# Optimization experiments

Hardware: AMD Instinct MI355X
Metric: run time of the kernel (lower is better)

Reference implementation:

```python
import jax, jax.numpy as jnp
import numpy as np

N = 100000

def _gcn_norm(edge_index, n):
    row, col = edge_index[0], edge_index[1]
    deg = jnp.zeros((n,), jnp.float32).at[col].add(1.0)
    dinv = jnp.where(deg > 0, jax.lax.rsqrt(jnp.maximum(deg, 1.0)), 0.0)
    return dinv[row] * dinv[col]


def _arma_conv(x, row, col, norm, init_w, w, root_w, bias):
    # x: [N, Fin]; init_w: [K, Fin, F]; w: [T-1, K, F, F]; root_w: [T, K, Fin, F]; bias: [T, K, 1, F]
    out = jnp.einsum('nf,kfg->kng', x, init_w)  # [K, N, F]
    T = root_w.shape[0]
    for t in range(T):
        if t > 0:
            out = jnp.einsum('kng,kgh->knh', out, w[t - 1])
        msg = out[:, row, :] * norm[None, :, None]          # [K, E, F] gather
        out = jnp.zeros_like(out).at[:, col, :].add(msg)    # scatter-add to targets
        out = out + jnp.einsum('nf,kfg->kng', x, root_w[t]) + bias[t]
        out = jax.nn.relu(out)
    return out.mean(axis=0)  # average over stacks K


def setup_inputs() -> dict:
    key = jax.random.key(0)
    ks = jax.random.split(key, 12)
    E, Fin, H, C, K = 1600000, 128, 64, 41, 2
    s = 0.1
    return {
        'x': jax.random.normal(ks[0], (N, Fin), jnp.float32),
        'edge_index': jax.random.randint(ks[1], (2, E), 0, N, jnp.int64),
        'w1_init': jax.random.normal(ks[2], (K, Fin, H), jnp.float32) * s,
        'w1': jax.random.normal(ks[3], (1, K, H, H), jnp.float32) * s,
        'w1_root': jax.random.normal(ks[4], (2, K, Fin, H), jnp.float32) * s,
        'b1': jax.random.normal(ks[5], (2, K, 1, H), jnp.float32) * s,
        'w2_init': jax.random.normal(ks[6], (K, H, C), jnp.float32) * s,
        'w2': jax.random.normal(ks[7], (1, K, C, C), jnp.float32) * s,
        'w2_root': jax.random.normal(ks[8], (2, K, H, C), jnp.float32) * s,
        'b2': jax.random.normal(ks[9], (2, K, 1, C), jnp.float32) * s,
    }


def reference(x, edge_index, w1_init, w1, w1_root, b1, w2_init, w2, w2_root, b2):
    row, col = edge_index[0], edge_index[1]
    norm = _gcn_norm(edge_index, N)
    h = jax.nn.relu(_arma_conv(x, row, col, norm, w1_init, w1, w1_root, b1))
    # F.dropout is identity in eval mode
    h = _arma_conv(h, row, col, norm, w2_init, w2, w2_root, b2)
    return jax.nn.log_softmax(h, axis=1)
```

## Files before the change

kernel.cpp:

```cpp
#include <hip/hip_runtime.h>
#include <math.h>

#define TPB 256
typedef unsigned short ushort_t;
typedef unsigned int uint_t;
typedef __attribute__((ext_vector_type(8))) short bf16x8;
typedef __attribute__((ext_vector_type(4))) float f32x4;

__device__ __forceinline__ float bf2f(ushort_t h) {
    return __uint_as_float(((uint_t)h) << 16);
}
__device__ __forceinline__ ushort_t f2bf(float f) {
    uint_t u = __float_as_uint(f);
    u += 0x7fff + ((u >> 16) & 1);
    return (ushort_t)(u >> 16);
}
__device__ __forceinline__ uint_t pack2(float x, float y) {
    return (uint_t)f2bf(x) | ((uint_t)f2bf(y) << 16);
}

__global__ void rank_kernel(const int* __restrict__ col, int* __restrict__ cnt,
                            int* __restrict__ pos, int E) {
    int e = blockIdx.x * blockDim.x + threadIdx.x;
    if (e < E) pos[e] = atomicAdd(&cnt[col[e]], 1);
}

__global__ void scan_block(const int* __restrict__ cnt, int* __restrict__ incl,
                           int* __restrict__ bsum, int N) {
    __shared__ int s[TPB];
    int i = blockIdx.x * TPB + threadIdx.x;
    s[threadIdx.x] = (i < N) ? cnt[i] : 0;
    __syncthreads();
    for (int d = 1; d < TPB; d <<= 1) {
        int t = (threadIdx.x >= d) ? s[threadIdx.x - d] : 0;
        __syncthreads();
        s[threadIdx.x] += t;
        __syncthreads();
    }
    if (i < N) incl[i] = s[threadIdx.x];
    if (threadIdx.x == TPB - 1) bsum[blockIdx.x] = s[TPB - 1];
}

__global__ void scan_bsums(int* __restrict__ bsum, int nb) {
    __shared__ int s[512];
    int t = threadIdx.x;
    int v = (t < nb) ? bsum[t] : 0;
    s[t] = v;
    __syncthreads();
    for (int d = 1; d < 512; d <<= 1) {
        int u = (t >= d) ? s[t - d] : 0;
        __syncthreads();
        s[t] += u;
        __syncthreads();
    }
    if (t < nb) bsum[t] = s[t] - v;
}

__global__ void finalize_csr(const int* __restrict__ incl, const int* __restrict__ bsum,
                             const int* __restrict__ cnt, int* __restrict__ rowstart,
                             float* __restrict__ dinv, int N) {
    int i = blockIdx.x * TPB + threadIdx.x;
    if (i < N) {
        rowstart[i + 1] = incl[i] + bsum[blockIdx.x];
        int d = cnt[i];
        dinv[i] = (d > 0) ? rsqrtf((float)d) : 0.0f;
    }
    if (i == 0) rowstart[0] = 0;
}

__global__ void fill_csr(const int* __restrict__ row, const int* __restrict__ col,
                         const int* __restrict__ rowstart, const int* __restrict__ pos,
                         int* __restrict__ srcidx, int E) {
    int e = blockIdx.x * blockDim.x + threadIdx.x;
    if (e < E) srcidx[rowstart[col[e]] + pos[e]] = row[e];
}

__global__ void cvt4_kernel(const float4* __restrict__ src, uint2* __restrict__ dst, int n4) {
    int i = blockIdx.x * blockDim.x + threadIdx.x;
    if (i < n4) {
        float4 v = src[i];
        dst[i] = make_uint2(pack2(v.x, v.y), pack2(v.z, v.w));
    }
}

#define SWZ_A 32768
#define SWZ_B 24576
#define SWZ_C 12288
#define SWZ_D 12288
__global__ void swz_all(const float* __restrict__ w1_init, const float* __restrict__ w1,
                        const float* __restrict__ w1_root, const float* __restrict__ w2_init,
                        const float* __restrict__ w2, const float* __restrict__ w2_root,
                        short* __restrict__ dst) {
    int idx = blockIdx.x * blockDim.x + threadIdx.x;
    int region, base, CH, CT;
    if (idx < SWZ_A)                          { region = 0; base = 0; CH = 4; CT = 8; }
    else if (idx < SWZ_A + SWZ_B)             { region = 1; base = SWZ_A; CH = 6; CT = 4; }
    else if (idx < SWZ_A + SWZ_B + SWZ_C)     { region = 2; base = SWZ_A + SWZ_B; CH = 2; CT = 6; }
    else if (idx < SWZ_A + SWZ_B + SWZ_C + SWZ_D)
                                              { region = 3; base = SWZ_A + SWZ_B + SWZ_C; CH = 4; CT = 3; }
    else return;
    int r = idx - base;
    int j = r & 7, ln = (r >> 3) & 63;
    int rest = r >> 9;
    int ct = rest % CT, c = (rest / CT) % CH, k = rest / (CT * CH);
    int col = ct * 16 + (ln & 15);
    int kl = (ln >> 4) * 8 + j;
    float v = 0.0f;
    if (region == 0) {
        int kk = c * 32 + kl;
        if (col < 64)       v = w1_init[((size_t)k * 128 + kk) * 64 + col];
        else                v = w1_root[((size_t)k * 128 + kk) * 64 + (col - 64)];
    } else if (region == 1) {
        if (c < 2) { int kk = c * 32 + kl;        v = w1[((size_t)k * 64 + kk) * 64 + col]; }
        else       { int kk = (c - 2) * 32 + kl;  v = w1_root[((size_t)(2 + k) * 128 + kk) * 64 + col]; }
    } else if (region == 2) {
        int kk = c * 32 + kl;
        if (col < 48) { if (col < 41)            v = w2_init[((size_t)k * 64 + kk) * 41 + col]; }
        else          { int c2 = col - 48; if (c2 < 41) v = w2_root[((size_t)k * 64 + kk) * 41 + c2]; }
    } else {
        if (c < 2) { int kk = c * 32 + kl;       if (kk < 41 && col < 41) v = w2[((size_t)k * 41 + kk) * 41 + col]; }
        else       { int kk = (c - 2) * 32 + kl; if (col < 41)            v = w2_root[((size_t)(2 + k) * 64 + kk) * 41 + col]; }
    }
    dst[(size_t)base + r] = (short)f2bf(v);
}

template<int CT, int CTA, int CH>
__global__ __launch_bounds__(256)
void gemm_t0(const ushort_t* __restrict__ s2, int s2s, const short* __restrict__ fragbuf,
             const float* __restrict__ biasB, int FB, int N,
             uint_t* __restrict__ pre, uint_t* __restrict__ outH) {
    constexpr int PP = (CT - CTA) * 8;
    constexpr int PA = CTA * 8;
    const int k = blockIdx.y;
    const int n0 = blockIdx.x * 128;
    const int t = threadIdx.x;
    const int w = t >> 6, lane = t & 63, quad = lane >> 4, lr = lane & 15;
    const short* fb = fragbuf + (size_t)k * CH * CT * 512;

    __shared__ short lds_b[CH * CT * 512];
    {
        constexpr int CHUNKS = CH * CT * 64;
#pragma unroll
        for (int i = 0; i < (CHUNKS + 255) / 256; ++i) {
            int idx = i * 256 + t;
            if (CHUNKS % 256 == 0 || idx < CHUNKS)
                *(bf16x8*)&lds_b[idx * 8] = *(const bf16x8*)&fb[(size_t)idx * 8];
        }
    }
    __syncthreads();

    int r0 = n0 + w * 32 + lr;
    int m0 = r0 < N ? r0 : N - 1;
    int m1 = (r0 + 16) < N ? (r0 + 16) : N - 1;

    f32x4 acc[2][CT];
#pragma unroll
    for (int rt = 0; rt < 2; ++rt)
#pragma unroll
        for (int ct = 0; ct < CT; ++ct) acc[rt][ct] = (f32x4){0.f, 0.f, 0.f, 0.f};

#pragma unroll
    for (int c = 0; c < CH; ++c) {
        int off = c * 32 + quad * 8;
        bf16x8 a0 = *(const bf16x8*)&s2[(size_t)m0 * s2s + off];
        bf16x8 a1 = *(const bf16x8*)&s2[(size_t)m1 * s2s + off];
#pragma unroll
        for (int ct = 0; ct < CT; ++ct) {
            bf16x8 b = *(const bf16x8*)&lds_b[((size_t)c * CT + ct) * 512 + lane * 8];
            acc[0][ct] = __builtin_amdgcn_mfma_f32_16x16x32_bf16(a0, b, acc[0][ct], 0, 0, 0);
            acc[1][ct] = __builtin_amdgcn_mfma_f32_16x16x32_bf16(a1, b, acc[1][ct], 0, 0, 0);
        }
    }

#pragma unroll
    for (int rt = 0; rt < 2; ++rt) {
#pragma unroll
        for (int i = 0; i < 4; ++i) {
            int n = n0 + w * 32 + rt * 16 + quad * 4 + i;
            if (n >= N) continue;
#pragma unroll
            for (int ct = 0; ct < CT; ++ct) {
                int col = ct * 16 + lr;
                float v = acc[rt][ct][i];
                if (ct >= CTA) {
                    int c2 = col - CTA * 16;
                    if (c2 < FB) v += biasB[(size_t)k * FB + c2];
                }
                float vn = __shfl_xor(v, 1);
                uint_t p = pack2(v, vn);
                uint_t p2 = __shfl_xor(p, 2);
                if (!(lr & 3)) {
                    if (ct < CTA) {
                        *(uint2*)&outH[((size_t)n * 2 + k) * PA + (col >> 1)] = make_uint2(p, p2);
                    } else {
                        int c2 = col - CTA * 16;
                        *(uint2*)&pre[((size_t)n * 2 + k) * PP + (c2 >> 1)] = make_uint2(p, p2);
                    }
                }
            }
        }
    }
}

__global__ __launch_bounds__(256)
void gemm_t1_l1(const ushort_t* __restrict__ s1, const ushort_t* __restrict__ xh,
                const short* __restrict__ fragbuf, const float* __restrict__ bias,
                int N, uint_t* __restrict__ hhU) {
    constexpr int CT = 4, CH = 6;
    const int n0 = blockIdx.x * 128;
    const int t = threadIdx.x;
    const int w = t >> 6, lane = t & 63, quad = lane >> 4, lr = lane & 15;

    __shared__ short lds_b[2 * CH * CT * 512];
    {
        constexpr int CHUNKS = 2 * CH * CT * 64;
#pragma unroll
        for (int i = 0; i < CHUNKS / 256; ++i) {
            int idx = i * 256 + t;
            *(bf16x8*)&lds_b[idx * 8] = *(const bf16x8*)&fragbuf[(size_t)idx * 8];
        }
    }
    __syncthreads();

    int r0 = n0 + w * 32 + lr;
    int m0 = r0 < N ? r0 : N - 1;
    int m1 = (r0 + 16) < N ? (r0 + 16) : N - 1;

    f32x4 acc[2][2][CT];
#pragma unroll
    for (int k = 0; k < 2; ++k)
#pragma unroll
        for (int rt = 0; rt < 2; ++rt)
#pragma unroll
            for (int ct = 0; ct < CT; ++ct) acc[k][rt][ct] = (f32x4){0.f, 0.f, 0.f, 0.f};

#pragma unroll
    for (int c = 0; c < CH; ++c) {
        bf16x8 a0[2], a1[2];
        if (c < 2) {
            int off = c * 32 + quad * 8;
#pragma unroll
            for (int k = 0; k < 2; ++k) {
                a0[k] = *(const bf16x8*)&s1[((size_t)m0 * 2 + k) * 64 + off];
                a1[k] = *(const bf16x8*)&s1[((size_t)m1 * 2 + k) * 64 + off];
            }
        } else {
            int off = (c - 2) * 32 + quad * 8;
            a0[0] = a0[1] = *(const bf16x8*)&xh[(size_t)m0 * 128 + off];
            a1[0] = a1[1] = *(const bf16x8*)&xh[(size_t)m1 * 128 + off];
        }
#pragma unroll
        for (int k = 0; k < 2; ++k) {
#pragma unroll
            for (int ct = 0; ct < CT; ++ct) {
                bf16x8 b = *(const bf16x8*)&lds_b[(((size_t)k * CH + c) * CT + ct) * 512 + lane * 8];
                acc[k][0][ct] = __builtin_amdgcn_mfma_f32_16x16x32_bf16(a0[k], b, acc[k][0][ct], 0, 0, 0);
                acc[k][1][ct] = __builtin_amdgcn_mfma_f32_16x16x32_bf16(a1[k], b, acc[k][1][ct], 0, 0, 0);
            }
        }
    }

#pragma unroll
    for (int rt = 0; rt < 2; ++rt) {
#pragma unroll
        for (int i = 0; i < 4; ++i) {
            int n = n0 + w * 32 + rt * 16 + quad * 4 + i;
            if (n >= N) continue;
#pragma unroll
            for (int ct = 0; ct < CT; ++ct) {
                int col = ct * 16 + lr;
                float v0 = fmaxf(acc[0][rt][ct][i] + bias[col], 0.0f);
                float v1 = fmaxf(acc[1][rt][ct][i] + bias[64 + col], 0.0f);
                float m = 0.5f * (v0 + v1);
                float mn = __shfl_xor(m, 1);
                uint_t p = pack2(m, mn);
                uint_t p2 = __shfl_xor(p, 2);
                if (!(lr & 3)) *(uint2*)&hhU[(size_t)n * 32 + (col >> 1)] = make_uint2(p, p2);
            }
        }
    }
}

__global__ __launch_bounds__(256)
void gemm_t1_l2(const ushort_t* __restrict__ s1, const ushort_t* __restrict__ hh,
                const short* __restrict__ fragbuf, const float* __restrict__ bias,
                int N, float* __restrict__ out) {
    constexpr int CT = 3, CH = 4;
    const int n0 = blockIdx.x * 128;
    const int t = threadIdx.x;
    const int w = t >> 6, lane = t & 63, quad = lane >> 4, lr = lane & 15;

    __shared__ short lds_b[2 * CH * CT * 512];
    {
        constexpr int CHUNKS = 2 * CH * CT * 64;
#pragma unroll
        for (int i = 0; i < CHUNKS / 256; ++i) {
            int idx = i * 256 + t;
            *(bf16x8*)&lds_b[idx * 8] = *(const bf16x8*)&fragbuf[(size_t)idx * 8];
        }
    }
    __syncthreads();

    int r0 = n0 + w * 32 + lr;
    int m0 = r0 < N ? r0 : N - 1;
    int m1 = (r0 + 16) < N ? (r0 + 16) : N - 1;

    f32x4 acc[2][2][CT];
#pragma unroll
    for (int k = 0; k < 2; ++k)
#pragma unroll
        for (int rt = 0; rt < 2; ++rt)
#pragma unroll
            for (int ct = 0; ct < CT; ++ct) acc[k][rt][ct] = (f32x4){0.f, 0.f, 0.f, 0.f};

#pragma unroll
    for (int c = 0; c < CH; ++c) {
        bf16x8 a0[2], a1[2];
        if (c < 2) {
            int off = c * 32 + quad * 8;
#pragma unroll
            for (int k = 0; k < 2; ++k) {
                a0[k] = *(const bf16x8*)&s1[((size_t)m0 * 2 + k) * 48 + off];
                a1[k] = *(const bf16x8*)&s1[((size_t)m1 * 2 + k) * 48 + off];
            }
        } else {
            int off = (c - 2) * 32 + quad * 8;
            a0[0] = a0[1] = *(const bf16x8*)&hh[(size_t)m0 * 64 + off];
            a1[0] = a1[1] = *(const bf16x8*)&hh[(size_t)m1 * 64 + off];
        }
#pragma unroll
        for (int k = 0; k < 2; ++k) {
#pragma unroll
            for (int ct = 0; ct < CT; ++ct) {
                bf16x8 b = *(const bf16x8*)&lds_b[(((size_t)k * CH + c) * CT + ct) * 512 + lane * 8];
                acc[k][0][ct] = __builtin_amdgcn_mfma_f32_16x16x32_bf16(a0[k], b, acc[k][0][ct], 0, 0, 0);
                acc[k][1][ct] = __builtin_amdgcn_mfma_f32_16x16x32_bf16(a1[k], b, acc[k][1][ct], 0, 0, 0);
            }
        }
    }

#pragma unroll
    for (int rt = 0; rt < 2; ++rt) {
#pragma unroll
        for (int i = 0; i < 4; ++i) {
            int n = n0 + w * 32 + rt * 16 + quad * 4 + i;
            float m[CT];
            float mx = -1e30f;
#pragma unroll
            for (int ct = 0; ct < CT; ++ct) {
                int col = ct * 16 + lr;
                float b0 = (col < 41) ? bias[col] : 0.0f;
                float b1v = (col < 41) ? bias[41 + col] : 0.0f;
                float v0 = fmaxf(acc[0][rt][ct][i] + b0, 0.0f);
                float v1 = fmaxf(acc[1][rt][ct][i] + b1v, 0.0f);
                m[ct] = 0.5f * (v0 + v1);
                if (col < 41) mx = fmaxf(mx, m[ct]);
            }
#pragma unroll
            for (int msk = 1; msk < 16; msk <<= 1) mx = fmaxf(mx, __shfl_xor(mx, msk));
            float s = 0.0f;
#pragma unroll
            for (int ct = 0; ct < CT; ++ct) {
                int col = ct * 16 + lr;
                if (col < 41) s += __expf(m[ct] - mx);
            }
#pragma unroll
            for (int msk = 1; msk < 16; msk <<= 1) s += __shfl_xor(s, msk);
            float ls = __logf(s);
            if (n < N) {
#pragma unroll
                for (int ct = 0; ct < CT; ++ct) {
                    int col = ct * 16 + lr;
                    if (col < 41) out[(size_t)n * 41 + col] = m[ct] - mx - ls;
                }
            }
        }
    }
}

template<int PAIRS>
__global__ __launch_bounds__(256)
void gather(const int* __restrict__ rowstart, const int* __restrict__ srcidx,
            const float* __restrict__ dinv, const uint_t* __restrict__ msg,
            const uint_t* __restrict__ pre, uint_t* __restrict__ outH, int N) {
    int gt = blockIdx.x * 256 + threadIdx.x;
    int n = gt >> 6, lane = gt & 63;
    if (n >= N) return;
    int k, pair;
    if (PAIRS == 32) { k = lane >> 5; pair = lane & 31; }
    else { k = lane / PAIRS; pair = lane - k * PAIRS; }
    if (k >= 2) return;
    int beg = rowstart[n], end = rowstart[n + 1];
    float dn = dinv[n];
    float ax = 0.0f, ay = 0.0f;
    int e = beg;
    for (; e + 7 < end; e += 8) {
        int s[8];
        float w[8];
        uint_t m[8];
#pragma unroll
        for (int j = 0; j < 8; ++j) s[j] = srcidx[e + j];
#pragma unroll
        for (int j = 0; j < 8; ++j) w[j] = dinv[s[j]];
#pragma unroll
        for (int j = 0; j < 8; ++j) m[j] = msg[((size_t)s[j] * 2 + k) * PAIRS + pair];
#pragma unroll
        for (int j = 0; j < 8; ++j) {
            float ww = w[j] * dn;
            ax = fmaf(bf2f((ushort_t)m[j]), ww, ax);
            ay = fmaf(bf2f((ushort_t)(m[j] >> 16)), ww, ay);
        }
    }
    if (e + 3 < end) {
        int s[4];
        float w[4];
        uint_t m[4];
#pragma unroll
        for (int j = 0; j < 4; ++j) s[j] = srcidx[e + j];
#pragma unroll
        for (int j = 0; j < 4; ++j) w[j] = dinv[s[j]];
#pragma unroll
        for (int j = 0; j < 4; ++j) m[j] = msg[((size_t)s[j] * 2 + k) * PAIRS + pair];
#pragma unroll
        for (int j = 0; j < 4; ++j) {
            float ww = w[j] * dn;
            ax = fmaf(bf2f((ushort_t)m[j]), ww, ax);
            ay = fmaf(bf2f((ushort_t)(m[j] >> 16)), ww, ay);
        }
        e += 4;
    }
    for (; e < end; ++e) {
        int s0 = srcidx[e];
        float ww = dinv[s0] * dn;
        uint_t m0 = msg[((size_t)s0 * 2 + k) * PAIRS + pair];
        ax = fmaf(bf2f((ushort_t)m0), ww, ax);
        ay = fmaf(bf2f((ushort_t)(m0 >> 16)), ww, ay);
    }
    size_t o = ((size_t)n * 2 + k) * PAIRS + pair;
    if (pre) {
        uint_t p = pre[o];
        ax = fmaxf(ax + bf2f((ushort_t)p), 0.0f);
        ay = fmaxf(ay + bf2f((ushort_t)(p >> 16)), 0.0f);
    }
    outH[o] = pack2(ax, ay);
}

extern "C" void kernel_launch(void* const* d_in, const int* in_sizes, int n_in,
                              void* d_out, int out_size, void* d_ws, size_t ws_size,
                              hipStream_t stream) {
    const float* x       = (const float*)d_in[0];
    const int*   ei      = (const int*)  d_in[1];
    const float* w1_init = (const float*)d_in[2];
    const float* w1      = (const float*)d_in[3];
    const float* w1_root = (const float*)d_in[4];
    const float* b1      = (const float*)d_in[5];
    const float* w2_init = (const float*)d_in[6];
    const float* w2      = (const float*)d_in[7];
    const float* w2_root = (const float*)d_in[8];
    const float* b2      = (const float*)d_in[9];

    const int Fin1 = 128;
    int N = in_sizes[0] / Fin1;
    int E = in_sizes[1] / 2;
    const int* row = ei;
    const int* col = ei + E;

    char* ws = (char*)d_ws;
    size_t off = 0;
    auto carve = [&](size_t bytes) -> void* {
        void* p = ws + off;
        off += (bytes + 255) & ~(size_t)255;
        return p;
    };
    int nblkN = (N + TPB - 1) / TPB;
    int*      cnt      = (int*)     carve((size_t)N * 4);
    int*      incl     = (int*)     carve((size_t)N * 4);
    int*      rowstart = (int*)     carve((size_t)(N + 1) * 4);
    int*      bsum     = (int*)     carve((size_t)nblkN * 4);
    float*    dinv     = (float*)   carve((size_t)N * 4);
    int*      pos      = (int*)     carve((size_t)E * 4);
    int*      srcidx   = (int*)     carve((size_t)E * 4);
    short*    swz      = (short*)   carve((size_t)(SWZ_A + SWZ_B + SWZ_C + SWZ_D) * 2);
    ushort_t* xh       = (ushort_t*)carve((size_t)N * 128 * 2);
    ushort_t* hh       = (ushort_t*)carve((size_t)N * 64 * 2);
    ushort_t* b16A     = (ushort_t*)carve((size_t)N * 2 * 64 * 2);
    ushort_t* b16B     = (ushort_t*)carve((size_t)N * 2 * 64 * 2);
    uint_t*   pre      = (uint_t*)  carve((size_t)N * 2 * 32 * 4);

    hipMemsetAsync(cnt, 0, (size_t)N * 4, stream);
    rank_kernel <<<(E + TPB - 1) / TPB, TPB, 0, stream>>>(col, cnt, pos, E);
    scan_block  <<<nblkN, TPB, 0, stream>>>(cnt, incl, bsum, N);
    scan_bsums  <<<1, 512, 0, stream>>>(bsum, nblkN);
    finalize_csr<<<nblkN, TPB, 0, stream>>>(incl, bsum, cnt, rowstart, dinv, N);
    fill_csr    <<<(E + TPB - 1) / TPB, TPB, 0, stream>>>(row, col, rowstart, pos, srcidx, E);

    int swztot = SWZ_A + SWZ_B + SWZ_C + SWZ_D;
    swz_all<<<(swztot + TPB - 1) / TPB, TPB, 0, stream>>>(w1_init, w1, w1_root,
                                                          w2_init, w2, w2_root, swz);
    int nx4 = N * 128 / 4;
    cvt4_kernel<<<(nx4 + TPB - 1) / TPB, TPB, 0, stream>>>((const float4*)x, (uint2*)xh, nx4);

    dim3 gg2((N + 127) / 128, 2);
    dim3 gg1((N + 127) / 128, 1);
    int ggb = (N * 64 + TPB - 1) / TPB;
    const short* swzA = swz;
    const short* swzB = swz + SWZ_A;
    const short* swzC = swz + SWZ_A + SWZ_B;
    const short* swzD = swz + SWZ_A + SWZ_B + SWZ_C;

    gemm_t0<8, 4, 4><<<gg2, TPB, 0, stream>>>(xh, 128, swzA, b1, 64, N, pre, (uint_t*)b16A);
    gather<32><<<ggb, TPB, 0, stream>>>(rowstart, srcidx, dinv, (const uint_t*)b16A,
                                        pre, (uint_t*)b16B, N);
    gather<32><<<ggb, TPB, 0, stream>>>(rowstart, srcidx, dinv, (const uint_t*)b16B,
                                        nullptr, (uint_t*)b16A, N);
    gemm_t1_l1<<<gg1, TPB, 0, stream>>>(b16A, xh, swzB, b1 + 2 * 64, N, (uint_t*)hh);

    gemm_t0<6, 3, 2><<<gg2, TPB, 0, stream>>>(hh, 64, swzC, b2, 41, N, pre, (uint_t*)b16A);
    gather<24><<<ggb, TPB, 0, stream>>>(rowstart, srcidx, dinv, (const uint_t*)b16A,
                                        pre, (uint_t*)b16B, N);
    gather<24><<<ggb, TPB, 0, stream>>>(rowstart, srcidx, dinv, (const uint_t*)b16B,
                                        nullptr, (uint_t*)b16A, N);
    gemm_t1_l2<<<gg1, TPB, 0, stream>>>(b16A, hh, swzD, b2 + 2 * 41, N, (float*)d_out);
}
```

Measured before the change: 606.2 us.

## Pad CSR rows to multiples of four and pre-scale messages by source dinv

Rows of the CSR adjacency are padded to a multiple of four with a dummy source index N that points at a zeroed tail row, so the gather can load indices as int4 and drop its scalar tail loops. The source-side normalisation dinv[s] is moved into the producer (the GEMM epilogue or the previous gather's output), which removes the per-edge dinv lookup and multiply. The per-edge rank is also stored as ushort, and the GEMMs hoist their A-operand global loads ahead of the LDS staging and get occupancy hints. In exchange it adds a padding kernel, extra memsets and a larger srcidx buffer. The ushort rank assumes in-degree below 65536, and the change in rounding order could shift bf16 results slightly.

```diff
diff --git a/kernel.cpp b/kernel.cpp
--- a/kernel.cpp
+++ b/kernel.cpp
@@ -20,16 +20,16 @@
 }
 
 __global__ void rank_kernel(const int* __restrict__ col, int* __restrict__ cnt,
-                            int* __restrict__ pos, int E) {
+                            unsigned short* __restrict__ pos, int E) {
     int e = blockIdx.x * blockDim.x + threadIdx.x;
-    if (e < E) pos[e] = atomicAdd(&cnt[col[e]], 1);
+    if (e < E) pos[e] = (unsigned short)atomicAdd(&cnt[col[e]], 1);
 }
 
 __global__ void scan_block(const int* __restrict__ cnt, int* __restrict__ incl,
                            int* __restrict__ bsum, int N) {
     __shared__ int s[TPB];
     int i = blockIdx.x * TPB + threadIdx.x;
-    s[threadIdx.x] = (i < N) ? cnt[i] : 0;
+    s[threadIdx.x] = (i < N) ? ((cnt[i] + 3) & ~3) : 0;
     __syncthreads();
     for (int d = 1; d < TPB; d <<= 1) {
         int t = (threadIdx.x >= d) ? s[threadIdx.x - d] : 0;
@@ -69,10 +69,18 @@
 }
 
 __global__ void fill_csr(const int* __restrict__ row, const int* __restrict__ col,
-                         const int* __restrict__ rowstart, const int* __restrict__ pos,
+                         const int* __restrict__ rowstart, const unsigned short* __restrict__ pos,
                          int* __restrict__ srcidx, int E) {
     int e = blockIdx.x * blockDim.x + threadIdx.x;
-    if (e < E) srcidx[rowstart[col[e]] + pos[e]] = row[e];
+    if (e < E) srcidx[rowstart[col[e]] + (int)pos[e]] = row[e];
+}
+
+__global__ void pad_csr(const int* __restrict__ rowstart, const int* __restrict__ cnt,
+                        int* __restrict__ srcidx, int N) {
+    int i = blockIdx.x * blockDim.x + threadIdx.x;
+    if (i >= N) return;
+    int b = rowstart[i] + cnt[i], en = rowstart[i + 1];
+    for (int e = b; e < en; ++e) srcidx[e] = N;
 }
 
 __global__ void cvt4_kernel(const float4* __restrict__ src, uint2* __restrict__ dst, int n4) {
@@ -125,10 +133,10 @@
 }
 
 template<int CT, int CTA, int CH>
-__global__ __launch_bounds__(256)
+__global__ __launch_bounds__(256, 4)
 void gemm_t0(const ushort_t* __restrict__ s2, int s2s, const short* __restrict__ fragbuf,
-             const float* __restrict__ biasB, int FB, int N,
-             uint_t* __restrict__ pre, uint_t* __restrict__ outH) {
+             const float* __restrict__ biasB, const float* __restrict__ dinv,
+             int FB, int N, uint_t* __restrict__ pre, uint_t* __restrict__ outH) {
     constexpr int PP = (CT - CTA) * 8;
     constexpr int PA = CTA * 8;
     const int k = blockIdx.y;
@@ -137,6 +145,18 @@
     const int w = t >> 6, lane = t & 63, quad = lane >> 4, lr = lane & 15;
     const short* fb = fragbuf + (size_t)k * CH * CT * 512;
 
+    int r0 = n0 + w * 32 + lr;
+    int m0 = r0 < N ? r0 : N - 1;
+    int m1 = (r0 + 16) < N ? (r0 + 16) : N - 1;
+
+    bf16x8 a0v[CH], a1v[CH];
+#pragma unroll
+    for (int c = 0; c < CH; ++c) {
+        int off = c * 32 + quad * 8;
+        a0v[c] = *(const bf16x8*)&s2[(size_t)m0 * s2s + off];
+        a1v[c] = *(const bf16x8*)&s2[(size_t)m1 * s2s + off];
+    }
+
     __shared__ short lds_b[CH * CT * 512];
     {
         constexpr int CHUNKS = CH * CT * 64;
@@ -149,10 +169,6 @@
     }
     __syncthreads();
 
-    int r0 = n0 + w * 32 + lr;
-    int m0 = r0 < N ? r0 : N - 1;
-    int m1 = (r0 + 16) < N ? (r0 + 16) : N - 1;
-
     f32x4 acc[2][CT];
 #pragma unroll
     for (int rt = 0; rt < 2; ++rt)
@@ -161,14 +177,11 @@
 
 #pragma unroll
     for (int c = 0; c < CH; ++c) {
-        int off = c * 32 + quad * 8;
-        bf16x8 a0 = *(const bf16x8*)&s2[(size_t)m0 * s2s + off];
-        bf16x8 a1 = *(const bf16x8*)&s2[(size_t)m1 * s2s + off];
 #pragma unroll
         for (int ct = 0; ct < CT; ++ct) {
             bf16x8 b = *(const bf16x8*)&lds_b[((size_t)c * CT + ct) * 512 + lane * 8];
-            acc[0][ct] = __builtin_amdgcn_mfma_f32_16x16x32_bf16(a0, b, acc[0][ct], 0, 0, 0);
-            acc[1][ct] = __builtin_amdgcn_mfma_f32_16x16x32_bf16(a1, b, acc[1][ct], 0, 0, 0);
+            acc[0][ct] = __builtin_amdgcn_mfma_f32_16x16x32_bf16(a0v[c], b, acc[0][ct], 0, 0, 0);
+            acc[1][ct] = __builtin_amdgcn_mfma_f32_16x16x32_bf16(a1v[c], b, acc[1][ct], 0, 0, 0);
         }
     }
 
@@ -178,11 +191,14 @@
         for (int i = 0; i < 4; ++i) {
             int n = n0 + w * 32 + rt * 16 + quad * 4 + i;
             if (n >= N) continue;
+            float dnv = dinv[n];
 #pragma unroll
             for (int ct = 0; ct < CT; ++ct) {
                 int col = ct * 16 + lr;
                 float v = acc[rt][ct][i];
-                if (ct >= CTA) {
+                if (ct < CTA) {
+                    v *= dnv;
+                } else {
                     int c2 = col - CTA * 16;
                     if (c2 < FB) v += biasB[(size_t)k * FB + c2];
                 }
@@ -202,7 +218,7 @@
     }
 }
 
-__global__ __launch_bounds__(256)
+__global__ __launch_bounds__(256, 3)
 void gemm_t1_l1(const ushort_t* __restrict__ s1, const ushort_t* __restrict__ xh,
                 const short* __restrict__ fragbuf, const float* __restrict__ bias,
                 int N, uint_t* __restrict__ hhU) {
@@ -211,6 +227,28 @@
     const int t = threadIdx.x;
     const int w = t >> 6, lane = t & 63, quad = lane >> 4, lr = lane & 15;
 
+    int r0 = n0 + w * 32 + lr;
+    int m0 = r0 < N ? r0 : N - 1;
+    int m1 = (r0 + 16) < N ? (r0 + 16) : N - 1;
+
+    bf16x8 s0a[2][2], s1a[2][2];
+    bf16x8 x0a[4], x1a[4];
+#pragma unroll
+    for (int c = 0; c < 2; ++c) {
+        int off = c * 32 + quad * 8;
+#pragma unroll
+        for (int kk = 0; kk < 2; ++kk) {
+            s0a[c][kk] = *(const bf16x8*)&s1[((size_t)m0 * 2 + kk) * 64 + off];
+            s1a[c][kk] = *(const bf16x8*)&s1[((size_t)m1 * 2 + kk) * 64 + off];
+        }
+    }
+#pragma unroll
+    for (int c = 0; c < 4; ++c) {
+        int off = c * 32 + quad * 8;
+        x0a[c] = *(const bf16x8*)&xh[(size_t)m0 * 128 + off];
+        x1a[c] = *(const bf16x8*)&xh[(size_t)m1 * 128 + off];
+    }
+
     __shared__ short lds_b[2 * CH * CT * 512];
     {
         constexpr int CHUNKS = 2 * CH * CT * 64;
@@ -222,10 +260,6 @@
     }
     __syncthreads();
 
-    int r0 = n0 + w * 32 + lr;
-    int m0 = r0 < N ? r0 : N - 1;
-    int m1 = (r0 + 16) < N ? (r0 + 16) : N - 1;
-
     f32x4 acc[2][2][CT];
 #pragma unroll
     for (int k = 0; k < 2; ++k)
@@ -236,26 +270,15 @@
 
 #pragma unroll
     for (int c = 0; c < CH; ++c) {
-        bf16x8 a0[2], a1[2];
-        if (c < 2) {
-            int off = c * 32 + quad * 8;
-#pragma unroll
-            for (int k = 0; k < 2; ++k) {
-                a0[k] = *(const bf16x8*)&s1[((size_t)m0 * 2 + k) * 64 + off];
-                a1[k] = *(const bf16x8*)&s1[((size_t)m1 * 2 + k) * 64 + off];
-            }
-        } else {
-            int off = (c - 2) * 32 + quad * 8;
-            a0[0] = a0[1] = *(const bf16x8*)&xh[(size_t)m0 * 128 + off];
-            a1[0] = a1[1] = *(const bf16x8*)&xh[(size_t)m1 * 128 + off];
-        }
 #pragma unroll
         for (int k = 0; k < 2; ++k) {
+            bf16x8 a0 = (c < 2) ? s0a[c][k] : x0a[c - 2];
+            bf16x8 a1 = (c < 2) ? s1a[c][k] : x1a[c - 2];
 #pragma unroll
             for (int ct = 0; ct < CT; ++ct) {
                 bf16x8 b = *(const bf16x8*)&lds_b[(((size_t)k * CH + c) * CT + ct) * 512 + lane * 8];
-                acc[k][0][ct] = __builtin_amdgcn_mfma_f32_16x16x32_bf16(a0[k], b, acc[k][0][ct], 0, 0, 0);
-                acc[k][1][ct] = __builtin_amdgcn_mfma_f32_16x16x32_bf16(a1[k], b, acc[k][1][ct], 0, 0, 0);
+                acc[k][0][ct] = __builtin_amdgcn_mfma_f32_16x16x32_bf16(a0, b, acc[k][0][ct], 0, 0, 0);
+                acc[k][1][ct] = __builtin_amdgcn_mfma_f32_16x16x32_bf16(a1, b, acc[k][1][ct], 0, 0, 0);
             }
         }
     }
@@ -281,7 +304,7 @@
     }
 }
 
-__global__ __launch_bounds__(256)
+__global__ __launch_bounds__(256, 3)
 void gemm_t1_l2(const ushort_t* __restrict__ s1, const ushort_t* __restrict__ hh,
                 const short* __restrict__ fragbuf, const float* __restrict__ bias,
                 int N, float* __restrict__ out) {
@@ -290,6 +313,28 @@
     const int t = threadIdx.x;
     const int w = t >> 6, lane = t & 63, quad = lane >> 4, lr = lane & 15;
 
+    int r0 = n0 + w * 32 + lr;
+    int m0 = r0 < N ? r0 : N - 1;
+    int m1 = (r0 + 16) < N ? (r0 + 16) : N - 1;
+
+    bf16x8 s0a[2][2], s1a[2][2];
+    bf16x8 h0a[2], h1a[2];
+#pragma unroll
+    for (int c = 0; c < 2; ++c) {
+        int off = c * 32 + quad * 8;
+#pragma unroll
+        for (int kk = 0; kk < 2; ++kk) {
+            s0a[c][kk] = *(const bf16x8*)&s1[((size_t)m0 * 2 + kk) * 48 + off];
+            s1a[c][kk] = *(const bf16x8*)&s1[((size_t)m1 * 2 + kk) * 48 + off];
+        }
+    }
+#pragma unroll
+    for (int c = 0; c < 2; ++c) {
+        int off = c * 32 + quad * 8;
+        h0a[c] = *(const bf16x8*)&hh[(size_t)m0 * 64 + off];
+        h1a[c] = *(const bf16x8*)&hh[(size_t)m1 * 64 + off];
+    }
+
     __shared__ short lds_b[2 * CH * CT * 512];
     {
         constexpr int CHUNKS = 2 * CH * CT * 64;
@@ -301,10 +346,6 @@
     }
     __syncthreads();
 
-    int r0 = n0 + w * 32 + lr;
-    int m0 = r0 < N ? r0 : N - 1;
-    int m1 = (r0 + 16) < N ? (r0 + 16) : N - 1;
-
     f32x4 acc[2][2][CT];
 #pragma unroll
     for (int k = 0; k < 2; ++k)
@@ -315,26 +356,15 @@
 
 #pragma unroll
     for (int c = 0; c < CH; ++c) {
-        bf16x8 a0[2], a1[2];
-        if (c < 2) {
-            int off = c * 32 + quad * 8;
-#pragma unroll
-            for (int k = 0; k < 2; ++k) {
-                a0[k] = *(const bf16x8*)&s1[((size_t)m0 * 2 + k) * 48 + off];
-                a1[k] = *(const bf16x8*)&s1[((size_t)m1 * 2 + k) * 48 + off];
-            }
-        } else {
-            int off = (c - 2) * 32 + quad * 8;
-            a0[0] = a0[1] = *(const bf16x8*)&hh[(size_t)m0 * 64 + off];
-            a1[0] = a1[1] = *(const bf16x8*)&hh[(size_t)m1 * 64 + off];
-        }
 #pragma unroll
         for (int k = 0; k < 2; ++k) {
+            bf16x8 a0 = (c < 2) ? s0a[c][k] : h0a[c - 2];
+            bf16x8 a1 = (c < 2) ? s1a[c][k] : h1a[c - 2];
 #pragma unroll
             for (int ct = 0; ct < CT; ++ct) {
                 bf16x8 b = *(const bf16x8*)&lds_b[(((size_t)k * CH + c) * CT + ct) * 512 + lane * 8];
-                acc[k][0][ct] = __builtin_amdgcn_mfma_f32_16x16x32_bf16(a0[k], b, acc[k][0][ct], 0, 0, 0);
-                acc[k][1][ct] = __builtin_amdgcn_mfma_f32_16x16x32_bf16(a1[k], b, acc[k][1][ct], 0, 0, 0);
+                acc[k][0][ct] = __builtin_amdgcn_mfma_f32_16x16x32_bf16(a0, b, acc[k][0][ct], 0, 0, 0);
+                acc[k][1][ct] = __builtin_amdgcn_mfma_f32_16x16x32_bf16(a1, b, acc[k][1][ct], 0, 0, 0);
             }
         }
     }
@@ -378,7 +408,7 @@
     }
 }
 
-template<int PAIRS>
+template<int PAIRS, bool SCALE_OUT>
 __global__ __launch_bounds__(256)
 void gather(const int* __restrict__ rowstart, const int* __restrict__ srcidx,
             const float* __restrict__ dinv, const uint_t* __restrict__ msg,
@@ -390,58 +420,54 @@
     if (PAIRS == 32) { k = lane >> 5; pair = lane & 31; }
     else { k = lane / PAIRS; pair = lane - k * PAIRS; }
     if (k >= 2) return;
+    const int STR = 2 * PAIRS;
+    const uint_t lo = (uint_t)(k * PAIRS + pair);
     int beg = rowstart[n], end = rowstart[n + 1];
     float dn = dinv[n];
-    float ax = 0.0f, ay = 0.0f;
+    size_t o = (size_t)n * STR + lo;
+    uint_t p = 0;
+    if (pre) p = pre[o];
+
+    float ax0 = 0.f, ax1 = 0.f, ay0 = 0.f, ay1 = 0.f;
     int e = beg;
-    for (; e + 7 < end; e += 8) {
-        int s[8];
-        float w[8];
-        uint_t m[8];
-#pragma unroll
-        for (int j = 0; j < 8; ++j) s[j] = srcidx[e + j];
-#pragma unroll
-        for (int j = 0; j < 8; ++j) w[j] = dinv[s[j]];
-#pragma unroll
-        for (int j = 0; j < 8; ++j) m[j] = msg[((size_t)s[j] * 2 + k) * PAIRS + pair];
-#pragma unroll
-        for (int j = 0; j < 8; ++j) {
-            float ww = w[j] * dn;
-            ax = fmaf(bf2f((ushort_t)m[j]), ww, ax);
-            ay = fmaf(bf2f((ushort_t)(m[j] >> 16)), ww, ay);
-        }
-    }
-    if (e + 3 < end) {
-        int s[4];
-        float w[4];
-        uint_t m[4];
-#pragma unroll
-        for (int j = 0; j < 4; ++j) s[j] = srcidx[e + j];
-#pragma unroll
-        for (int j = 0; j < 4; ++j) w[j] = dinv[s[j]];
-#pragma unroll
-        for (int j = 0; j < 4; ++j) m[j] = msg[((size_t)s[j] * 2 + k) * PAIRS + pair];
-#pragma unroll
-        for (int j = 0; j < 4; ++j) {
-            float ww = w[j] * dn;
-            ax = fmaf(bf2f((ushort_t)m[j]), ww, ax);
-            ay = fmaf(bf2f((ushort_t)(m[j] >> 16)), ww, ay);
-        }
-        e += 4;
-    }
-    for (; e < end; ++e) {
-        int s0 = srcidx[e];
-        float ww = dinv[s0] * dn;
-        uint_t m0 = msg[((size_t)s0 * 2 + k) * PAIRS + pair];
-        ax = fmaf(bf2f((ushort_t)m0), ww, ax);
-        ay = fmaf(bf2f((ushort_t)(m0 >> 16)), ww, ay);
-    }
-    size_t o = ((size_t)n * 2 + k) * PAIRS + pair;
+    for (; e + 8 <= end; e += 8) {
+        int4 sa = *(const int4*)&srcidx[e];
+        int4 sb = *(const int4*)&srcidx[e + 4];
+        uint_t m0 = msg[(uint_t)(sa.x * STR) + lo];
+        uint_t m1 = msg[(uint_t)(sa.y * STR) + lo];
+        uint_t m2 = msg[(uint_t)(sa.z * STR) + lo];
+        uint_t m3 = msg[(uint_t)(sa.w * STR) + lo];
+        uint_t m4 = msg[(uint_t)(sb.x * STR) + lo];
+        uint_t m5 = msg[(uint_t)(sb.y * STR) + lo];
+        uint_t m6 = msg[(uint_t)(sb.z * STR) + lo];
+        uint_t m7 = msg[(uint_t)(sb.w * STR) + lo];
+        ax0 += __uint_as_float(m0 << 16); ay0 += __uint_as_float(m0 & 0xffff0000u);
+        ax1 += __uint_as_float(m1 << 16); ay1 += __uint_as_float(m1 & 0xffff0000u);
+        ax0 += __uint_as_float(m2 << 16); ay0 += __uint_as_float(m2 & 0xffff0000u);
+        ax1 += __uint_as_float(m3 << 16); ay1 += __uint_as_float(m3 & 0xffff0000u);
+        ax0 += __uint_as_float(m4 << 16); ay0 += __uint_as_float(m4 & 0xffff0000u);
+        ax1 += __uint_as_float(m5 << 16); ay1 += __uint_as_float(m5 & 0xffff0000u);
+        ax0 += __uint_as_float(m6 << 16); ay0 += __uint_as_float(m6 & 0xffff0000u);
+        ax1 += __uint_as_float(m7 << 16); ay1 += __uint_as_float(m7 & 0xffff0000u);
+    }
+    if (e < end) {
+        int4 sa = *(const int4*)&srcidx[e];
+        uint_t m0 = msg[(uint_t)(sa.x * STR) + lo];
+        uint_t m1 = msg[(uint_t)(sa.y * STR) + lo];
+        uint_t m2 = msg[(uint_t)(sa.z * STR) + lo];
+        uint_t m3 = msg[(uint_t)(sa.w * STR) + lo];
+        ax0 += __uint_as_float(m0 << 16); ay0 += __uint_as_float(m0 & 0xffff0000u);
+        ax1 += __uint_as_float(m1 << 16); ay1 += __uint_as_float(m1 & 0xffff0000u);
+        ax0 += __uint_as_float(m2 << 16); ay0 += __uint_as_float(m2 & 0xffff0000u);
+        ax1 += __uint_as_float(m3 << 16); ay1 += __uint_as_float(m3 & 0xffff0000u);
+    }
+    float ax = (ax0 + ax1) * dn;
+    float ay = (ay0 + ay1) * dn;
     if (pre) {
-        uint_t p = pre[o];
         ax = fmaxf(ax + bf2f((ushort_t)p), 0.0f);
         ay = fmaxf(ay + bf2f((ushort_t)(p >> 16)), 0.0f);
     }
+    if (SCALE_OUT) { ax *= dn; ay *= dn; }
     outH[o] = pack2(ax, ay);
 }
 
@@ -478,20 +504,24 @@
     int*      rowstart = (int*)     carve((size_t)(N + 1) * 4);
     int*      bsum     = (int*)     carve((size_t)nblkN * 4);
     float*    dinv     = (float*)   carve((size_t)N * 4);
-    int*      pos      = (int*)     carve((size_t)E * 4);
-    int*      srcidx   = (int*)     carve((size_t)E * 4);
+    unsigned short* pos = (unsigned short*)carve((size_t)E * 2);
+    int*      srcidx   = (int*)     carve((size_t)(E + 3 * (size_t)N + 64) * 4);
     short*    swz      = (short*)   carve((size_t)(SWZ_A + SWZ_B + SWZ_C + SWZ_D) * 2);
     ushort_t* xh       = (ushort_t*)carve((size_t)N * 128 * 2);
     ushort_t* hh       = (ushort_t*)carve((size_t)N * 64 * 2);
-    ushort_t* b16A     = (ushort_t*)carve((size_t)N * 2 * 64 * 2);
-    ushort_t* b16B     = (ushort_t*)carve((size_t)N * 2 * 64 * 2);
+    ushort_t* b16A     = (ushort_t*)carve((size_t)N * 2 * 64 * 2 + 256);
+    ushort_t* b16B     = (ushort_t*)carve((size_t)N * 2 * 64 * 2 + 256);
     uint_t*   pre      = (uint_t*)  carve((size_t)N * 2 * 32 * 4);
+
+    hipMemsetAsync((char*)b16A + (size_t)N * 256, 0, 256, stream);
+    hipMemsetAsync((char*)b16B + (size_t)N * 256, 0, 256, stream);
 
     hipMemsetAsync(cnt, 0, (size_t)N * 4, stream);
     rank_kernel <<<(E + TPB - 1) / TPB, TPB, 0, stream>>>(col, cnt, pos, E);
     scan_block  <<<nblkN, TPB, 0, stream>>>(cnt, incl, bsum, N);
     scan_bsums  <<<1, 512, 0, stream>>>(bsum, nblkN);
     finalize_csr<<<nblkN, TPB, 0, stream>>>(incl, bsum, cnt, rowstart, dinv, N);
+    pad_csr     <<<nblkN, TPB, 0, stream>>>(rowstart, cnt, srcidx, N);
     fill_csr    <<<(E + TPB - 1) / TPB, TPB, 0, stream>>>(row, col, rowstart, pos, srcidx, E);
 
     int swztot = SWZ_A + SWZ_B + SWZ_C + SWZ_D;
@@ -508,17 +538,20 @@
     const short* swzC = swz + SWZ_A + SWZ_B;
     const short* swzD = swz + SWZ_A + SWZ_B + SWZ_C;
 
-    gemm_t0<8, 4, 4><<<gg2, TPB, 0, stream>>>(xh, 128, swzA, b1, 64, N, pre, (uint_t*)b16A);
-    gather<32><<<ggb, TPB, 0, stream>>>(rowstart, srcidx, dinv, (const uint_t*)b16A,
-                                        pre, (uint_t*)b16B, N);
-    gather<32><<<ggb, TPB, 0, stream>>>(rowstart, srcidx, dinv, (const uint_t*)b16B,
-                                        nullptr, (uint_t*)b16A, N);
+    gemm_t0<8, 4, 4><<<gg2, TPB, 0, stream>>>(xh, 128, swzA, b1, dinv, 64, N, pre, (uint_t*)b16A);
+    gather<32, true ><<<ggb, TPB, 0, stream>>>(rowstart, srcidx, dinv, (const uint_t*)b16A,
+                                               pre, (uint_t*)b16B, N);
+    gather<32, false><<<ggb, TPB, 0, stream>>>(rowstart, srcidx, dinv, (const uint_t*)b16B,
+                                               nullptr, (uint_t*)b16A, N);
     gemm_t1_l1<<<gg1, TPB, 0, stream>>>(b16A, xh, swzB, b1 + 2 * 64, N, (uint_t*)hh);
 
-    gemm_t0<6, 3, 2><<<gg2, TPB, 0, stream>>>(hh, 64, swzC, b2, 41, N, pre, (uint_t*)b16A);
-    gather<24><<<ggb, TPB, 0, stream>>>(rowstart, srcidx, dinv, (const uint_t*)b16A,
-                                        pre, (uint_t*)b16B, N);
-    gather<24><<<ggb, TPB, 0, stream>>>(rowstart, srcidx, dinv, (const uint_t*)b16B,
-                                        nullptr, (uint_t*)b16A, N);
+    hipMemsetAsync((char*)b16A + (size_t)N * 192, 0, 192, stream);
+    hipMemsetAsync((char*)b16B + (size_t)N * 192, 0, 192, stream);
+
+    gemm_t0<6, 3, 2><<<gg2, TPB, 0, stream>>>(hh, 64, swzC, b2, dinv, 41, N, pre, (uint_t*)b16A);
+    gather<24, true ><<<ggb, TPB, 0, stream>>>(rowstart, srcidx, dinv, (const uint_t*)b16A,
+                                               pre, (uint_t*)b16B, N);
+    gather<24, false><<<ggb, TPB, 0, stream>>>(rowstart, srcidx, dinv, (const uint_t*)b16B,
+                                               nullptr, (uint_t*)b16A, N);
     gemm_t1_l2<<<gg1, TPB, 0, stream>>>(b16A, hh, swzD, b2 + 2 * 41, N, (float*)d_out);
 }
```

Result: faster. 563.0 us (-7.1%).
